# Optimization experiments

Measured on AMD Instinct MI355X. Metric: run time of the kernel, lower is better.

The kernel has to match this reference:

```python
import jax, jax.numpy as jnp
import numpy as np

N = 50000          # nodes
E = 1250000        # edges (avg degree 25)
EMBED = 64
HIDS = [64, 64, 64]
EDGE_DIM = 7       # 1 + 6
VOCAB = 5 ** 8     # 390625
NEG_SLOPE = 0.01   # F.leaky_relu default


def setup_inputs() -> dict:
    key = jax.random.key(0)
    ks = jax.random.split(key, 14)
    L = len(HIDS)
    x = jax.random.randint(ks[0], (N,), 0, VOCAB)
    edge_index = jax.random.randint(ks[1], (2, E), 0, N)
    edge_attr = jax.random.normal(ks[2], (E, EDGE_DIM), dtype=jnp.float32)
    emb = jax.random.normal(ks[3], (VOCAB, EMBED), dtype=jnp.float32) * 0.02
    # all layers have in = out = 64, so params are stacked along layer axis
    lin1_w = jax.random.normal(ks[4], (L, EMBED + EDGE_DIM, HIDS[0]), dtype=jnp.float32) * 0.1
    att_l = jax.random.normal(ks[5], (L, HIDS[0]), dtype=jnp.float32) * 0.1
    att_r = jax.random.normal(ks[6], (L, EMBED), dtype=jnp.float32) * 0.1
    lin2_w = jax.random.normal(ks[7], (L, HIDS[0], HIDS[0]), dtype=jnp.float32) * 0.1
    gbias = jax.random.normal(ks[8], (L, HIDS[0]), dtype=jnp.float32) * 0.01
    d_cat = int(np.sum(HIDS)) + EMBED  # 256
    fc1_w = jax.random.normal(ks[9], (d_cat, 20), dtype=jnp.float32) * 0.05
    fc1_b = jax.random.normal(ks[10], (20,), dtype=jnp.float32) * 0.01
    fc2_w = jax.random.normal(ks[11], (20, 1), dtype=jnp.float32) * 0.1
    fc2_b = jax.random.normal(ks[12], (1,), dtype=jnp.float32) * 0.01
    return {"x": x, "edge_index": edge_index, "edge_attr": edge_attr, "emb": emb,
            "lin1_w": lin1_w, "att_l": att_l, "att_r": att_r, "lin2_w": lin2_w,
            "gbias": gbias, "fc1_w": fc1_w, "fc1_b": fc1_b, "fc2_w": fc2_w, "fc2_b": fc2_b}


def _gate_conv(h, src, dst, edge_attr, w1, al, ar, w2, b):
    # message from source j -> target i; attention softmax over edges sharing a target
    xj = jnp.concatenate([h[src], edge_attr], axis=-1)            # [E, in+7]
    xj = jax.nn.leaky_relu(xj @ w1, NEG_SLOPE)                    # [E, out]
    alpha = jax.nn.leaky_relu(jnp.sum(xj * al, -1) + jnp.sum(h[dst] * ar, -1), NEG_SLOPE)
    amax = jax.ops.segment_max(alpha, dst, num_segments=N)        # [N]
    ea = jnp.exp(alpha - amax[dst])                               # [E]
    denom = jax.ops.segment_sum(ea, dst, num_segments=N)          # [N]
    a = ea / (denom[dst] + 1e-16)
    msg = (xj @ w2) * a[:, None]                                  # [E, out]
    return jax.ops.segment_sum(msg, dst, num_segments=N) + b      # [N, out]


def reference(x, edge_index, edge_attr, emb, lin1_w, att_l, att_r, lin2_w,
              gbias, fc1_w, fc1_b, fc2_w, fc2_b):
    src, dst = edge_index[0], edge_index[1]
    h = emb[x]                                                    # [N, EMBED]
    feats = [h]
    for l in range(len(HIDS)):
        h = jax.nn.relu(_gate_conv(h, src, dst, edge_attr,
                                   lin1_w[l], att_l[l], att_r[l], lin2_w[l], gbias[l]))
        feats.append(h)
    hcat = jnp.concatenate(feats, axis=-1)                        # [N, 256]
    z = jax.nn.relu(hcat @ fc1_w + fc1_b)
    out = jax.nn.sigmoid(z @ fc2_w + fc2_b)
    return out.squeeze(-1)                                        # [N]
```

## Files before the change

### kernel.cpp

```cpp
#include <hip/hip_runtime.h>
#include <math.h>

#define NEG 0.01f

typedef _Float16 f16;
typedef f16 h2 __attribute__((ext_vector_type(2)));

__device__ __forceinline__ float lrelu(float x) { return x > 0.f ? x : NEG * x; }

__device__ __forceinline__ h2 lrelu2(h2 x) {
    h2 y = x * (f16)0.01f;
    return __builtin_elementwise_max(x, y);
}

__device__ __forceinline__ float q16_allsum(float v) {
    int x;
    x = __builtin_amdgcn_update_dpp(0, __float_as_int(v), 0xB1, 0xF, 0xF, true);  v += __int_as_float(x);
    x = __builtin_amdgcn_update_dpp(0, __float_as_int(v), 0x4E, 0xF, 0xF, true);  v += __int_as_float(x);
    x = __builtin_amdgcn_update_dpp(0, __float_as_int(v), 0x124, 0xF, 0xF, true); v += __int_as_float(x);
    x = __builtin_amdgcn_update_dpp(0, __float_as_int(v), 0x128, 0xF, 0xF, true); v += __int_as_float(x);
    return v;
}

__device__ __forceinline__ float x16_32_sum(float v) {
    v += __int_as_float(__builtin_amdgcn_ds_swizzle(__float_as_int(v), 0x401F));
    v += __shfl_xor(v, 32, 64);
    return v;
}

__global__ void k_pre(int* __restrict__ deg, int N,
                      const float* __restrict__ lin1, const float* __restrict__ attl,
                      uint4* __restrict__ wpack, uint4* __restrict__ rec, int E) {
    int i = blockIdx.x * blockDim.x + threadIdx.x;
    if (i < N) deg[i] = 0;
    if (i < 48) {
        int l = i >> 4, t = i & 15;
        const float* wb  = lin1 + (size_t)l * 71 * 64 + 64 * 64;
        const float* alp = attl + l * 64;
        unsigned int u[20];
#pragma unroll
        for (int j = 0; j < 4; j++) {
            int f = 4 * t + j;
            h2 a = { (f16)wb[f],       (f16)wb[64 + f]  }; u[j]      = __builtin_bit_cast(unsigned int, a);
            h2 b = { (f16)wb[128 + f], (f16)wb[192 + f] }; u[4 + j]  = __builtin_bit_cast(unsigned int, b);
            h2 c = { (f16)wb[256 + f], (f16)wb[320 + f] }; u[8 + j]  = __builtin_bit_cast(unsigned int, c);
            h2 d = { (f16)wb[384 + f], (f16)0.f         }; u[12 + j] = __builtin_bit_cast(unsigned int, d);
        }
        h2 e0 = { (f16)alp[4 * t],     (f16)alp[4 * t + 1] }; u[16] = __builtin_bit_cast(unsigned int, e0);
        h2 e1 = { (f16)alp[4 * t + 2], (f16)alp[4 * t + 3] }; u[17] = __builtin_bit_cast(unsigned int, e1);
        u[18] = 0; u[19] = 0;
        uint4* o = wpack + (size_t)i * 5;
        o[0] = make_uint4(u[0],  u[1],  u[2],  u[3]);
        o[1] = make_uint4(u[4],  u[5],  u[6],  u[7]);
        o[2] = make_uint4(u[8],  u[9],  u[10], u[11]);
        o[3] = make_uint4(u[12], u[13], u[14], u[15]);
        o[4] = make_uint4(u[16], u[17], u[18], u[19]);
    } else if (i >= 48 && i < 112) {
        rec[E + i - 48] = make_uint4(0, 0, 0, 0);
    }
}

__global__ __launch_bounds__(256) void k_count_gemm0(
    const int* __restrict__ dst, int* __restrict__ deg, int* __restrict__ rank,
    int E, int nbC,
    const int* __restrict__ x, const float* __restrict__ emb,
    const float* __restrict__ lin1, const float* __restrict__ ar,
    f16* __restrict__ g, float* __restrict__ r_out, float* __restrict__ hcat, int N)
{
    __shared__ __align__(16) float sA[64][36];
    __shared__ __align__(16) float sB[64 * 64];
    __shared__ float sar[64];
    int tid = threadIdx.x;
    if ((int)blockIdx.x < nbC) {
        int e = (blockIdx.x * 256 + tid) * 4;
        if (e + 3 < E) {
            int4 d = *(const int4*)(dst + e);
            int r0 = atomicAdd(&deg[d.x], 1);
            int r1 = atomicAdd(&deg[d.y], 1);
            int r2 = atomicAdd(&deg[d.z], 1);
            int r3 = atomicAdd(&deg[d.w], 1);
            *(int4*)(rank + e) = make_int4(r0, r1, r2, r3);
        } else {
            for (int k = 0; k < 4; k++)
                if (e + k < E) rank[e + k] = atomicAdd(&deg[dst[e + k]], 1);
        }
        return;
    }
    int row0 = ((int)blockIdx.x - nbC) * 32;

    {
        const float4* b4 = (const float4*)lin1;
        float4* s4 = (float4*)sB;
        for (int i = tid; i < 1024; i += 256) s4[i] = b4[i];
    }
    if (tid < 64) sar[tid] = ar[tid];

#pragma unroll
    for (int pass = 0; pass < 2; ++pass) {
        int nl = pass * 16 + (tid & 15);
        int k4 = (tid >> 4) * 4;
        int n = row0 + nl; bool ok = n < N; if (!ok) n = N - 1;
        float4 v = *(const float4*)(emb + (size_t)x[n] * 64 + k4);
        sA[k4 + 0][nl] = v.x; sA[k4 + 1][nl] = v.y;
        sA[k4 + 2][nl] = v.z; sA[k4 + 3][nl] = v.w;
        if (ok) *(float4*)(hcat + (size_t)n * 256 + k4) = v;
    }
    __syncthreads();

    int tr = tid >> 4, tc = tid & 15;
    int r0 = tr * 2, c0 = tc * 4;
    float acc[2][4];
#pragma unroll
    for (int i = 0; i < 2; i++)
#pragma unroll
        for (int j = 0; j < 4; j++) acc[i][j] = 0.f;

#pragma unroll 4
    for (int k = 0; k < 64; ++k) {
        float4 b4 = *(const float4*)(sB + k * 64 + c0);
        float2 a0 = *(const float2*)&sA[k][r0];
#pragma unroll
        for (int j = 0; j < 4; j++) {
            float bj = (&b4.x)[j];
            acc[0][j] += a0.x * bj; acc[1][j] += a0.y * bj;
        }
    }

#pragma unroll
    for (int i = 0; i < 2; i++) {
        int n = row0 + r0 + i;
        if (n < N) {
            uint2 gw;
            gw.x = __builtin_bit_cast(unsigned int, __builtin_amdgcn_cvt_pkrtz(acc[i][0], acc[i][1]));
            gw.y = __builtin_bit_cast(unsigned int, __builtin_amdgcn_cvt_pkrtz(acc[i][2], acc[i][3]));
            *(uint2*)(g + (size_t)n * 64 + c0) = gw;
        }
    }
    if (tid < 32) {
        int n = row0 + tid;
        if (n < N) {
            float racc = 0.f;
#pragma unroll
            for (int k = 0; k < 64; k++) racc += sA[k][tid] * sar[k];
            r_out[n] = racc;
        }
    }
}

__global__ __launch_bounds__(256) void k_scan_part(const int* __restrict__ deg,
                                                   int* __restrict__ bsum, int n) {
    __shared__ int sh[256];
    int b = blockIdx.x, t = threadIdx.x;
    int i0 = b * 1024 + t * 4;
    int s = 0;
    if (i0 + 3 < n) { int4 v = *(const int4*)(deg + i0); s = v.x + v.y + v.z + v.w; }
    else { for (int k = 0; k < 4; k++) if (i0 + k < n) s += deg[i0 + k]; }
    sh[t] = s; __syncthreads();
    for (int d = 128; d > 0; d >>= 1) { if (t < d) sh[t] += sh[t + d]; __syncthreads(); }
    if (t == 0) bsum[b] = sh[0];
}

__global__ __launch_bounds__(256) void k_scan_out(const int* __restrict__ deg,
                                                  const int* __restrict__ bsum,
                                                  int* __restrict__ off, int nb, int n) {
    __shared__ int sb[256];
    __shared__ int sh[256];
    int b = blockIdx.x, t = threadIdx.x;
    int v = (t < nb) ? bsum[t] : 0;
    sb[t] = v; __syncthreads();
    for (int d = 1; d < 256; d <<= 1) {
        int u = (t >= d) ? sb[t - d] : 0;
        __syncthreads(); sb[t] += u; __syncthreads();
    }
    int base = (b == 0) ? 0 : sb[b - 1];
    if (b == 0 && t == 0) off[n] = sb[255];
    int i0 = b * 1024 + t * 4;
    int4 v4 = make_int4(0, 0, 0, 0);
    if (i0 + 3 < n) v4 = *(const int4*)(deg + i0);
    else {
        v4.x = (i0     < n) ? deg[i0]     : 0;
        v4.y = (i0 + 1 < n) ? deg[i0 + 1] : 0;
        v4.z = (i0 + 2 < n) ? deg[i0 + 2] : 0;
        v4.w = (i0 + 3 < n) ? deg[i0 + 3] : 0;
    }
    int s = v4.x + v4.y + v4.z + v4.w;
    sh[t] = s; __syncthreads();
    for (int d = 1; d < 256; d <<= 1) {
        int u = (t >= d) ? sh[t - d] : 0;
        __syncthreads(); sh[t] += u; __syncthreads();
    }
    int ex = base + sh[t] - s;
    if (i0     < n) off[i0]     = ex;
    if (i0 + 1 < n) off[i0 + 1] = ex + v4.x;
    if (i0 + 2 < n) off[i0 + 2] = ex + v4.x + v4.y;
    if (i0 + 3 < n) off[i0 + 3] = ex + v4.x + v4.y + v4.z;
}

__global__ void k_fill(const int* __restrict__ src, const int* __restrict__ dst,
                       const float* __restrict__ eattr, const int* __restrict__ off,
                       const int* __restrict__ rank, uint4* __restrict__ rec, int E) {
    int e = (blockIdx.x * 256 + threadIdx.x) * 2;
    if (e >= E) return;
    bool two = (e + 1 < E);
#pragma unroll
    for (int k = 0; k < 2; k++) {
        if (k == 1 && !two) break;
        int ee = e + k;
        int slot = off[dst[ee]] + rank[ee];
        const float* ap = eattr + (size_t)ee * 7;
        float a0 = ap[0], a1 = ap[1], a2 = ap[2], a3 = ap[3], a4 = ap[4], a5 = ap[5], a6 = ap[6];
        uint4 rv;
        h2 p01 = { (f16)a0, (f16)a1 };
        h2 p23 = { (f16)a2, (f16)a3 };
        h2 p45 = { (f16)a4, (f16)a5 };
        rv.x = __builtin_bit_cast(unsigned int, p01);
        rv.y = __builtin_bit_cast(unsigned int, p23);
        rv.z = __builtin_bit_cast(unsigned int, p45);
        unsigned int a6b = (unsigned int)__builtin_bit_cast(unsigned short, (f16)a6);
        rv.w = a6b | ((unsigned int)src[ee] << 16);
        rec[slot] = rv;
    }
}

__global__ __launch_bounds__(256) void k_gemm2g1(
    float* __restrict__ hc,
    const float* __restrict__ W2, const float* __restrict__ bias,
    const float* __restrict__ W1n, const float* __restrict__ arn,
    f16* __restrict__ g, float* __restrict__ r_out, int N)
{
    __shared__ __align__(16) float sA[64][68];
    __shared__ __align__(16) float sB[64 * 64];
    __shared__ float sar[64];
    int tid = threadIdx.x, row0 = blockIdx.x * 64;

    {
        const float4* b4 = (const float4*)W2;
        float4* s4 = (float4*)sB;
        for (int i = tid; i < 1024; i += 256) s4[i] = b4[i];
    }
    if (tid < 64) sar[tid] = arn[tid];

#pragma unroll
    for (int pass = 0; pass < 4; ++pass) {
        int nl = pass * 16 + (tid & 15);
        int k4 = (tid >> 4) * 4;
        int n = row0 + nl; if (n >= N) n = N - 1;
        float4 v = *(const float4*)(hc + (size_t)n * 256 + k4);
        sA[k4 + 0][nl] = v.x; sA[k4 + 1][nl] = v.y;
        sA[k4 + 2][nl] = v.z; sA[k4 + 3][nl] = v.w;
    }
    __syncthreads();

    int tr = tid >> 4, tc = tid & 15;
    int r0 = tr * 4, c0 = tc * 4;
    float acc[4][4];
#pragma unroll
    for (int i = 0; i < 4; i++)
#pragma unroll
        for (int j = 0; j < 4; j++) acc[i][j] = 0.f;

#pragma unroll 4
    for (int k = 0; k < 64; ++k) {
        float4 b4 = *(const float4*)(sB + k * 64 + c0);
        float4 a0 = *(const float4*)&sA[k][r0];
#pragma unroll
        for (int j = 0; j < 4; j++) {
            float bj = (&b4.x)[j];
            acc[0][j] += a0.x * bj; acc[1][j] += a0.y * bj;
            acc[2][j] += a0.z * bj; acc[3][j] += a0.w * bj;
        }
    }

    float4 bv = *(const float4*)(bias + c0);
#pragma unroll
    for (int i = 0; i < 4; i++) {
        acc[i][0] = fmaxf(acc[i][0] + bv.x, 0.f);
        acc[i][1] = fmaxf(acc[i][1] + bv.y, 0.f);
        acc[i][2] = fmaxf(acc[i][2] + bv.z, 0.f);
        acc[i][3] = fmaxf(acc[i][3] + bv.w, 0.f);
        int n = row0 + r0 + i;
        if (n < N) *(float4*)(hc + (size_t)n * 256 + c0) =
            make_float4(acc[i][0], acc[i][1], acc[i][2], acc[i][3]);
    }
    __syncthreads();

    {
        const float4* b4 = (const float4*)W1n;
        float4* s4 = (float4*)sB;
        for (int i = tid; i < 1024; i += 256) s4[i] = b4[i];
    }
#pragma unroll
    for (int i = 0; i < 4; i++)
#pragma unroll
        for (int j = 0; j < 4; j++) sA[c0 + j][r0 + i] = acc[i][j];
    __syncthreads();

#pragma unroll
    for (int i = 0; i < 4; i++)
#pragma unroll
        for (int j = 0; j < 4; j++) acc[i][j] = 0.f;

#pragma unroll 4
    for (int k = 0; k < 64; ++k) {
        float4 b4 = *(const float4*)(sB + k * 64 + c0);
        float4 a0 = *(const float4*)&sA[k][r0];
#pragma unroll
        for (int j = 0; j < 4; j++) {
            float bj = (&b4.x)[j];
            acc[0][j] += a0.x * bj; acc[1][j] += a0.y * bj;
            acc[2][j] += a0.z * bj; acc[3][j] += a0.w * bj;
        }
    }

#pragma unroll
    for (int i = 0; i < 4; i++) {
        int n = row0 + r0 + i;
        if (n < N) {
            uint2 gw;
            gw.x = __builtin_bit_cast(unsigned int, __builtin_amdgcn_cvt_pkrtz(acc[i][0], acc[i][1]));
            gw.y = __builtin_bit_cast(unsigned int, __builtin_amdgcn_cvt_pkrtz(acc[i][2], acc[i][3]));
            *(uint2*)(g + (size_t)n * 64 + c0) = gw;
        }
    }
    if (tid < 64) {
        int n = row0 + tid;
        if (n < N) {
            float racc = 0.f;
#pragma unroll
            for (int k = 0; k < 64; k++) racc += sA[k][tid] * sar[k];
            r_out[n] = racc;
        }
    }
}

struct ConvW {
    h2 w01[4], w23[4], w45[4], w6_[4];
    h2 al01, al23;
};

__device__ __forceinline__ void edge_math(uint4 rv, uint2 gv, bool valid, float ri,
                                          const ConvW& W, float4& s, float& den) {
    h2 a01 = __builtin_bit_cast(h2, rv.x);
    h2 a23 = __builtin_bit_cast(h2, rv.y);
    h2 a45 = __builtin_bit_cast(h2, rv.z);
    h2 a6p = __builtin_bit_cast(h2, rv.w & 0xFFFFu);
    h2 g01 = __builtin_bit_cast(h2, gv.x);
    h2 g23 = __builtin_bit_cast(h2, gv.y);

    float c0 = __builtin_amdgcn_fdot2(a01, W.w01[0],
               __builtin_amdgcn_fdot2(a23, W.w23[0],
               __builtin_amdgcn_fdot2(a45, W.w45[0],
               __builtin_amdgcn_fdot2(a6p, W.w6_[0], 0.f, false), false), false), false);
    float c1 = __builtin_amdgcn_fdot2(a01, W.w01[1],
               __builtin_amdgcn_fdot2(a23, W.w23[1],
               __builtin_amdgcn_fdot2(a45, W.w45[1],
               __builtin_amdgcn_fdot2(a6p, W.w6_[1], 0.f, false), false), false), false);
    float c2 = __builtin_amdgcn_fdot2(a01, W.w01[2],
               __builtin_amdgcn_fdot2(a23, W.w23[2],
               __builtin_amdgcn_fdot2(a45, W.w45[2],
               __builtin_amdgcn_fdot2(a6p, W.w6_[2], 0.f, false), false), false), false);
    float c3 = __builtin_amdgcn_fdot2(a01, W.w01[3],
               __builtin_amdgcn_fdot2(a23, W.w23[3],
               __builtin_amdgcn_fdot2(a45, W.w45[3],
               __builtin_amdgcn_fdot2(a6p, W.w6_[3], 0.f, false), false), false), false);

    h2 x01 = lrelu2(g01 + __builtin_amdgcn_cvt_pkrtz(c0, c1));
    h2 x23 = lrelu2(g23 + __builtin_amdgcn_cvt_pkrtz(c2, c3));
    float p = __builtin_amdgcn_fdot2(x01, W.al01,
              __builtin_amdgcn_fdot2(x23, W.al23, 0.f, false), false);
    p = q16_allsum(p);
    float alpha = lrelu(p + ri);
    float w = valid ? __expf(alpha) : 0.f;
    s.x += w * (float)x01.x; s.y += w * (float)x01.y;
    s.z += w * (float)x23.x; s.w += w * (float)x23.y;
    den += w;
}

__global__ __launch_bounds__(256) void k_conv(
    const int* __restrict__ off, const uint4* __restrict__ rec,
    const f16* __restrict__ g, const float* __restrict__ r,
    const uint4* __restrict__ wpack, float* __restrict__ aggdst, int N)
{
    int lane = threadIdx.x & 63;
    int wid  = threadIdx.x >> 6;
    int node = blockIdx.x * 4 + wid;
    if (node >= N) return;
    int q = lane >> 4, l16 = lane & 15;

    ConvW W;
    {
        const uint4* wp = wpack + l16 * 5;
        uint4 v0 = wp[0], v1 = wp[1], v2 = wp[2], v3 = wp[3], v4 = wp[4];
        W.w01[0] = __builtin_bit_cast(h2, v0.x); W.w01[1] = __builtin_bit_cast(h2, v0.y);
        W.w01[2] = __builtin_bit_cast(h2, v0.z); W.w01[3] = __builtin_bit_cast(h2, v0.w);
        W.w23[0] = __builtin_bit_cast(h2, v1.x); W.w23[1] = __builtin_bit_cast(h2, v1.y);
        W.w23[2] = __builtin_bit_cast(h2, v1.z); W.w23[3] = __builtin_bit_cast(h2, v1.w);
        W.w45[0] = __builtin_bit_cast(h2, v2.x); W.w45[1] = __builtin_bit_cast(h2, v2.y);
        W.w45[2] = __builtin_bit_cast(h2, v2.z); W.w45[3] = __builtin_bit_cast(h2, v2.w);
        W.w6_[0] = __builtin_bit_cast(h2, v3.x); W.w6_[1] = __builtin_bit_cast(h2, v3.y);
        W.w6_[2] = __builtin_bit_cast(h2, v3.z); W.w6_[3] = __builtin_bit_cast(h2, v3.w);
        W.al01   = __builtin_bit_cast(h2, v4.x); W.al23   = __builtin_bit_cast(h2, v4.y);
    }

    float ri = r[node];
    int e0 = off[node], e1 = off[node + 1];
    const f16* gq = g + 4 * l16;

    float4 s = make_float4(0.f, 0.f, 0.f, 0.f);
    float den = 0.f;
    if (e0 < e1) {
        const uint4* rp = rec + e0 + q;
        uint4 ra = rp[0], rb = rp[4], rc = rp[8], rd = rp[12];
        uint2 ga = *(const uint2*)(gq + (size_t)(ra.w >> 16) * 64);
        uint2 gb = *(const uint2*)(gq + (size_t)(rb.w >> 16) * 64);
        uint2 gc = *(const uint2*)(gq + (size_t)(rc.w >> 16) * 64);
        uint2 gd = *(const uint2*)(gq + (size_t)(rd.w >> 16) * 64);
        uint4 na = rp[16], nb = rp[20], nc = rp[24], nd = rp[28];
        for (int e = e0; e < e1; e += 16) {
            uint2 gna = *(const uint2*)(gq + (size_t)(na.w >> 16) * 64);
            uint2 gnb = *(const uint2*)(gq + (size_t)(nb.w >> 16) * 64);
            uint2 gnc = *(const uint2*)(gq + (size_t)(nc.w >> 16) * 64);
            uint2 gnd = *(const uint2*)(gq + (size_t)(nd.w >> 16) * 64);
            rp += 16;
            uint4 ma = rp[16], mb = rp[20], mc = rp[24], md = rp[28];
            bool va = (e + q)      < e1, vb = (e + 4 + q)  < e1;
            bool vc = (e + 8 + q)  < e1, vd = (e + 12 + q) < e1;
            edge_math(ra, ga, va, ri, W, s, den);
            edge_math(rb, gb, vb, ri, W, s, den);
            edge_math(rc, gc, vc, ri, W, s, den);
            edge_math(rd, gd, vd, ri, W, s, den);
            ra = na; rb = nb; rc = nc; rd = nd;
            ga = gna; gb = gnb; gc = gnc; gd = gnd;
            na = ma; nb = mb; nc = mc; nd = md;
        }
    }
    s.x = x16_32_sum(s.x); s.y = x16_32_sum(s.y);
    s.z = x16_32_sum(s.z); s.w = x16_32_sum(s.w);
    den = x16_32_sum(den);
    float inv = 1.f / (den + 1e-16f);
    if (q == 0) {
        float4 o = make_float4(s.x * inv, s.y * inv, s.z * inv, s.w * inv);
        *(float4*)(aggdst + (size_t)node * 256 + 4 * l16) = o;
    }
}

__global__ __launch_bounds__(256) void k_gemm2head(
    const float* __restrict__ hcat,
    const float* __restrict__ W2, const float* __restrict__ bias,
    const float* __restrict__ f1w, const float* __restrict__ f1b,
    const float* __restrict__ f2w, const float* __restrict__ f2b,
    float* __restrict__ out, int N)
{
    __shared__ __align__(16) float sA[64][130];
    __shared__ __align__(16) float sBW[5120];
    int tid = threadIdx.x, row0 = blockIdx.x * 128;

    {
        const float4* b4 = (const float4*)W2;
        float4* s4 = (float4*)sBW;
        for (int i = tid; i < 1024; i += 256) s4[i] = b4[i];
    }
#pragma unroll
    for (int pass = 0; pass < 8; ++pass) {
        int nl = pass * 16 + (tid & 15);
        int k4 = (tid >> 4) * 4;
        int n = row0 + nl; if (n >= N) n = N - 1;
        float4 v = *(const float4*)(hcat + (size_t)n * 256 + 192 + k4);
        sA[k4 + 0][nl] = v.x; sA[k4 + 1][nl] = v.y;
        sA[k4 + 2][nl] = v.z; sA[k4 + 3][nl] = v.w;
    }
    __syncthreads();

    int tr = tid >> 4, tc = tid & 15;
    int r0 = tr * 8, c0 = tc * 4;
    float acc[8][4];
#pragma unroll
    for (int i = 0; i < 8; i++)
#pragma unroll
        for (int j = 0; j < 4; j++) acc[i][j] = 0.f;

#pragma unroll 4
    for (int k = 0; k < 64; ++k) {
        float4 b4 = *(const float4*)(sBW + k * 64 + c0);
        float4 a0 = *(const float4*)&sA[k][r0];
        float4 a1 = *(const float4*)&sA[k][r0 + 4];
#pragma unroll
        for (int j = 0; j < 4; j++) {
            float bj = (&b4.x)[j];
            acc[0][j] += a0.x * bj; acc[1][j] += a0.y * bj;
            acc[2][j] += a0.z * bj; acc[3][j] += a0.w * bj;
            acc[4][j] += a1.x * bj; acc[5][j] += a1.y * bj;
            acc[6][j] += a1.z * bj; acc[7][j] += a1.w * bj;
        }
    }

    float4 fw[5];
    {
        const float4* w4 = (const float4*)f1w;
#pragma unroll
        for (int i2 = 0; i2 < 5; i2++) fw[i2] = w4[tid + i2 * 256];
    }
    __syncthreads();

    float* sO = &sA[0][0];
    float4 bv = *(const float4*)(bias + c0);
#pragma unroll
    for (int i = 0; i < 8; i++) {
        acc[i][0] = fmaxf(acc[i][0] + bv.x, 0.f);
        acc[i][1] = fmaxf(acc[i][1] + bv.y, 0.f);
        acc[i][2] = fmaxf(acc[i][2] + bv.z, 0.f);
        acc[i][3] = fmaxf(acc[i][3] + bv.w, 0.f);
        int rr = r0 + i;
        sO[rr * 65 + c0 + 0] = acc[i][0];
        sO[rr * 65 + c0 + 1] = acc[i][1];
        sO[rr * 65 + c0 + 2] = acc[i][2];
        sO[rr * 65 + c0 + 3] = acc[i][3];
    }
    {
        float4* sw4 = (float4*)sBW;
#pragma unroll
        for (int i2 = 0; i2 < 5; i2++) sw4[tid + i2 * 256] = fw[i2];
    }
    __syncthreads();

    int rloc = tid >> 1;
    int half = tid & 1;
    int n = row0 + rloc;
    int nn = (n < N) ? n : N - 1;
    float z[20];
#pragma unroll
    for (int j = 0; j < 20; j++) z[j] = 0.f;
    const float4* hr = (const float4*)(hcat + (size_t)nn * 256);
    if (half == 0) {
        for (int k4 = 0; k4 < 32; k4++) {
            float4 h = hr[k4];
            const float* wr = sBW + k4 * 80;
#pragma unroll
            for (int j = 0; j < 20; j++)
                z[j] += h.x * wr[j] + h.y * wr[20 + j] + h.z * wr[40 + j] + h.w * wr[60 + j];
        }
    } else {
        for (int k4 = 32; k4 < 48; k4++) {
            float4 h = hr[k4];
            const float* wr = sBW + k4 * 80;
#pragma unroll
            for (int j = 0; j < 20; j++)
                z[j] += h.x * wr[j] + h.y * wr[20 + j] + h.z * wr[40 + j] + h.w * wr[60 + j];
        }
        for (int k = 0; k < 64; k += 2) {
            float hx = sO[rloc * 65 + k], hy = sO[rloc * 65 + k + 1];
            const float* wr = sBW + (192 + k) * 20;
#pragma unroll
            for (int j = 0; j < 20; j++)
                z[j] += hx * wr[j] + hy * wr[20 + j];
        }
    }
#pragma unroll
    for (int j = 0; j < 20; j++) z[j] += __shfl_xor(z[j], 1, 64);
    if (half == 0 && n < N) {
        float o = f2b[0];
#pragma unroll
        for (int j = 0; j < 20; j++) {
            float zj = z[j] + f1b[j];
            o += fmaxf(zj, 0.f) * f2w[j];
        }
        out[n] = 1.f / (1.f + __expf(-o));
    }
}

extern "C" void kernel_launch(void* const* d_in, const int* in_sizes, int n_in,
                              void* d_out, int out_size, void* d_ws, size_t ws_size,
                              hipStream_t stream) {
    const int*   x     = (const int*)d_in[0];
    const int*   eidx  = (const int*)d_in[1];
    const float* eattr = (const float*)d_in[2];
    const float* emb   = (const float*)d_in[3];
    const float* lin1  = (const float*)d_in[4];
    const float* attl  = (const float*)d_in[5];
    const float* attr_ = (const float*)d_in[6];
    const float* lin2  = (const float*)d_in[7];
    const float* gbias = (const float*)d_in[8];
    const float* f1w   = (const float*)d_in[9];
    const float* f1b   = (const float*)d_in[10];
    const float* f2w   = (const float*)d_in[11];
    const float* f2b   = (const float*)d_in[12];
    float* out = (float*)d_out;

    int N = in_sizes[0];
    int E = in_sizes[1] / 2;
    const int* src = eidx;
    const int* dst = eidx + E;

    char* p = (char*)d_ws;
    auto alloc = [&](size_t bytes) { void* q = (void*)p; p += (bytes + 255) & ~(size_t)255; return q; };
    float* hcat = (float*)alloc((size_t)N * 256 * 4);
    f16*   g    = (f16*)alloc((size_t)N * 64 * 2);
    float* r    = (float*)alloc((size_t)N * 4);
    int*   off  = (int*)alloc((size_t)(N + 1) * 4);
    int*   deg  = (int*)alloc((size_t)N * 4);
    int*   rank = (int*)alloc((size_t)E * 4);
    int*   bsum = (int*)alloc(256 * 4);
    uint4* rec  = (uint4*)alloc((size_t)(E + 64) * 16);
    uint4* wpack = (uint4*)alloc((size_t)48 * 5 * 16);

    int nbs   = (N + 1023) / 1024;
    int nbC   = ((E + 3) / 4 + 255) / 256;
    int nbG0  = (N + 31) / 32;
    int nbF   = ((E + 1) / 2 + 255) / 256;
    int nbg64 = (N + 63) / 64;
    int nbg128 = (N + 127) / 128;
    int nbc   = (N + 3) / 4;

    k_pre<<<(N + 255) / 256, 256, 0, stream>>>(deg, N, lin1, attl, wpack, rec, E);
    k_count_gemm0<<<nbC + nbG0, 256, 0, stream>>>(dst, deg, rank, E, nbC,
                                                  x, emb, lin1, attr_, g, r, hcat, N);
    k_scan_part<<<nbs, 256, 0, stream>>>(deg, bsum, N);
    k_scan_out<<<nbs, 256, 0, stream>>>(deg, bsum, off, nbs, N);
    k_fill<<<nbF, 256, 0, stream>>>(src, dst, eattr, off, rank, rec, E);

    k_conv<<<nbc, 256, 0, stream>>>(off, rec, g, r, wpack, hcat + 64, N);
    for (int l = 0; l < 2; l++) {
        k_gemm2g1<<<nbg64, 256, 0, stream>>>(hcat + 64 * (l + 1),
                                             lin2 + (size_t)l * 4096, gbias + l * 64,
                                             lin1 + (size_t)(l + 1) * 71 * 64,
                                             attr_ + (l + 1) * 64, g, r, N);
        k_conv<<<nbc, 256, 0, stream>>>(off, rec, g, r,
                                        wpack + (size_t)(l + 1) * 80,
                                        hcat + 64 * (l + 2), N);
    }
    k_gemm2head<<<nbg128, 256, 0, stream>>>(hcat, lin2 + 2 * 4096, gbias + 128,
                                            f1w, f1b, f2w, f2b, out, N);
}
```

Baseline: 514.0 us.

## Compute per-edge lin1 with MFMA in conv instead of node-level precompute

```diff
diff --git a/kernel.cpp b/kernel.cpp
--- a/kernel.cpp
+++ b/kernel.cpp
@@ -5,13 +5,10 @@
 
 typedef _Float16 f16;
 typedef f16 h2 __attribute__((ext_vector_type(2)));
+typedef f16 h4 __attribute__((ext_vector_type(4)));
+typedef float f32x4 __attribute__((ext_vector_type(4)));
 
 __device__ __forceinline__ float lrelu(float x) { return x > 0.f ? x : NEG * x; }
-
-__device__ __forceinline__ h2 lrelu2(h2 x) {
-    h2 y = x * (f16)0.01f;
-    return __builtin_elementwise_max(x, y);
-}
 
 __device__ __forceinline__ float q16_allsum(float v) {
     int x;
@@ -29,47 +26,39 @@
 }
 
 __global__ void k_pre(int* __restrict__ deg, int N,
-                      const float* __restrict__ lin1, const float* __restrict__ attl,
-                      uint4* __restrict__ wpack, uint4* __restrict__ rec, int E) {
+                      const float* __restrict__ lin1, uint2* __restrict__ wpack2,
+                      uint4* __restrict__ rec, int E) {
     int i = blockIdx.x * blockDim.x + threadIdx.x;
     if (i < N) deg[i] = 0;
-    if (i < 48) {
-        int l = i >> 4, t = i & 15;
-        const float* wb  = lin1 + (size_t)l * 71 * 64 + 64 * 64;
-        const float* alp = attl + l * 64;
-        unsigned int u[20];
-#pragma unroll
-        for (int j = 0; j < 4; j++) {
-            int f = 4 * t + j;
-            h2 a = { (f16)wb[f],       (f16)wb[64 + f]  }; u[j]      = __builtin_bit_cast(unsigned int, a);
-            h2 b = { (f16)wb[128 + f], (f16)wb[192 + f] }; u[4 + j]  = __builtin_bit_cast(unsigned int, b);
-            h2 c = { (f16)wb[256 + f], (f16)wb[320 + f] }; u[8 + j]  = __builtin_bit_cast(unsigned int, c);
-            h2 d = { (f16)wb[384 + f], (f16)0.f         }; u[12 + j] = __builtin_bit_cast(unsigned int, d);
-        }
-        h2 e0 = { (f16)alp[4 * t],     (f16)alp[4 * t + 1] }; u[16] = __builtin_bit_cast(unsigned int, e0);
-        h2 e1 = { (f16)alp[4 * t + 2], (f16)alp[4 * t + 3] }; u[17] = __builtin_bit_cast(unsigned int, e1);
-        u[18] = 0; u[19] = 0;
-        uint4* o = wpack + (size_t)i * 5;
-        o[0] = make_uint4(u[0],  u[1],  u[2],  u[3]);
-        o[1] = make_uint4(u[4],  u[5],  u[6],  u[7]);
-        o[2] = make_uint4(u[8],  u[9],  u[10], u[11]);
-        o[3] = make_uint4(u[12], u[13], u[14], u[15]);
-        o[4] = make_uint4(u[16], u[17], u[18], u[19]);
-    } else if (i >= 48 && i < 112) {
-        rec[E + i - 48] = make_uint4(0, 0, 0, 0);
-    }
-}
-
-__global__ __launch_bounds__(256) void k_count_gemm0(
+    if (i < 3840) {
+        int lane = i & 63, rest = i >> 6;
+        int nb = rest & 3, rest2 = rest >> 2;
+        int s = rest2 % 5, L = rest2 / 5;
+        int f  = nb * 16 + (lane & 15);
+        int kb = s * 16 + ((lane >> 4) << 2);
+        const float* W = lin1 + (size_t)L * 71 * 64;
+        float v0 = (kb + 0 < 71) ? W[(kb + 0) * 64 + f] : 0.f;
+        float v1 = (kb + 1 < 71) ? W[(kb + 1) * 64 + f] : 0.f;
+        float v2 = (kb + 2 < 71) ? W[(kb + 2) * 64 + f] : 0.f;
+        float v3 = (kb + 3 < 71) ? W[(kb + 3) * 64 + f] : 0.f;
+        h2 p01 = { (f16)v0, (f16)v1 };
+        h2 p23 = { (f16)v2, (f16)v3 };
+        uint2 u;
+        u.x = __builtin_bit_cast(unsigned int, p01);
+        u.y = __builtin_bit_cast(unsigned int, p23);
+        wpack2[i] = u;
+    }
+    if (i >= 3840 && i < 3904) rec[E + i - 3840] = make_uint4(0, 0, 0, 0);
+}
+
+__global__ __launch_bounds__(256) void k_count_h0(
     const int* __restrict__ dst, int* __restrict__ deg, int* __restrict__ rank,
     int E, int nbC,
     const int* __restrict__ x, const float* __restrict__ emb,
-    const float* __restrict__ lin1, const float* __restrict__ ar,
-    f16* __restrict__ g, float* __restrict__ r_out, float* __restrict__ hcat, int N)
+    const float* __restrict__ ar0,
+    f16* __restrict__ h16, float* __restrict__ r_out,
+    float* __restrict__ hcat, int N)
 {
-    __shared__ __align__(16) float sA[64][36];
-    __shared__ __align__(16) float sB[64 * 64];
-    __shared__ float sar[64];
     int tid = threadIdx.x;
     if ((int)blockIdx.x < nbC) {
         int e = (blockIdx.x * 256 + tid) * 4;
@@ -86,65 +75,20 @@
         }
         return;
     }
-    int row0 = ((int)blockIdx.x - nbC) * 32;
-
-    {
-        const float4* b4 = (const float4*)lin1;
-        float4* s4 = (float4*)sB;
-        for (int i = tid; i < 1024; i += 256) s4[i] = b4[i];
-    }
-    if (tid < 64) sar[tid] = ar[tid];
-
-#pragma unroll
-    for (int pass = 0; pass < 2; ++pass) {
-        int nl = pass * 16 + (tid & 15);
-        int k4 = (tid >> 4) * 4;
-        int n = row0 + nl; bool ok = n < N; if (!ok) n = N - 1;
-        float4 v = *(const float4*)(emb + (size_t)x[n] * 64 + k4);
-        sA[k4 + 0][nl] = v.x; sA[k4 + 1][nl] = v.y;
-        sA[k4 + 2][nl] = v.z; sA[k4 + 3][nl] = v.w;
-        if (ok) *(float4*)(hcat + (size_t)n * 256 + k4) = v;
-    }
-    __syncthreads();
-
-    int tr = tid >> 4, tc = tid & 15;
-    int r0 = tr * 2, c0 = tc * 4;
-    float acc[2][4];
-#pragma unroll
-    for (int i = 0; i < 2; i++)
-#pragma unroll
-        for (int j = 0; j < 4; j++) acc[i][j] = 0.f;
-
-#pragma unroll 4
-    for (int k = 0; k < 64; ++k) {
-        float4 b4 = *(const float4*)(sB + k * 64 + c0);
-        float2 a0 = *(const float2*)&sA[k][r0];
-#pragma unroll
-        for (int j = 0; j < 4; j++) {
-            float bj = (&b4.x)[j];
-            acc[0][j] += a0.x * bj; acc[1][j] += a0.y * bj;
-        }
-    }
-
-#pragma unroll
-    for (int i = 0; i < 2; i++) {
-        int n = row0 + r0 + i;
-        if (n < N) {
-            uint2 gw;
-            gw.x = __builtin_bit_cast(unsigned int, __builtin_amdgcn_cvt_pkrtz(acc[i][0], acc[i][1]));
-            gw.y = __builtin_bit_cast(unsigned int, __builtin_amdgcn_cvt_pkrtz(acc[i][2], acc[i][3]));
-            *(uint2*)(g + (size_t)n * 64 + c0) = gw;
-        }
-    }
-    if (tid < 32) {
-        int n = row0 + tid;
-        if (n < N) {
-            float racc = 0.f;
-#pragma unroll
-            for (int k = 0; k < 64; k++) racc += sA[k][tid] * sar[k];
-            r_out[n] = racc;
-        }
-    }
+    int idx = ((int)blockIdx.x - nbC) * 256 + tid;
+    int node = idx >> 4, sub = idx & 15;
+    if (node >= N) return;
+    int j4 = sub * 4;
+    float4 em = *(const float4*)(emb + (size_t)x[node] * 64 + j4);
+    *(float4*)(hcat + (size_t)node * 256 + j4) = em;
+    uint2 hw;
+    hw.x = __builtin_bit_cast(unsigned int, __builtin_amdgcn_cvt_pkrtz(em.x, em.y));
+    hw.y = __builtin_bit_cast(unsigned int, __builtin_amdgcn_cvt_pkrtz(em.z, em.w));
+    *(uint2*)(h16 + (size_t)node * 64 + j4) = hw;
+    float part = em.x * ar0[j4] + em.y * ar0[j4 + 1]
+               + em.z * ar0[j4 + 2] + em.w * ar0[j4 + 3];
+    part = q16_allsum(part);
+    if (sub == 0) r_out[node] = part;
 }
 
 __global__ __launch_bounds__(256) void k_scan_part(const int* __restrict__ deg,
@@ -222,11 +166,11 @@
     }
 }
 
-__global__ __launch_bounds__(256) void k_gemm2g1(
+__global__ __launch_bounds__(256) void k_gemm2h(
     float* __restrict__ hc,
     const float* __restrict__ W2, const float* __restrict__ bias,
-    const float* __restrict__ W1n, const float* __restrict__ arn,
-    f16* __restrict__ g, float* __restrict__ r_out, int N)
+    const float* __restrict__ arn,
+    f16* __restrict__ h16, float* __restrict__ r_out, int N)
 {
     __shared__ __align__(16) float sA[64][68];
     __shared__ __align__(16) float sB[64 * 64];
@@ -279,168 +223,111 @@
         acc[i][2] = fmaxf(acc[i][2] + bv.z, 0.f);
         acc[i][3] = fmaxf(acc[i][3] + bv.w, 0.f);
         int n = row0 + r0 + i;
-        if (n < N) *(float4*)(hc + (size_t)n * 256 + c0) =
-            make_float4(acc[i][0], acc[i][1], acc[i][2], acc[i][3]);
-    }
-    __syncthreads();
-
-    {
-        const float4* b4 = (const float4*)W1n;
-        float4* s4 = (float4*)sB;
-        for (int i = tid; i < 1024; i += 256) s4[i] = b4[i];
-    }
-#pragma unroll
-    for (int i = 0; i < 4; i++)
-#pragma unroll
-        for (int j = 0; j < 4; j++) sA[c0 + j][r0 + i] = acc[i][j];
-    __syncthreads();
-
-#pragma unroll
-    for (int i = 0; i < 4; i++)
-#pragma unroll
-        for (int j = 0; j < 4; j++) acc[i][j] = 0.f;
-
-#pragma unroll 4
-    for (int k = 0; k < 64; ++k) {
-        float4 b4 = *(const float4*)(sB + k * 64 + c0);
-        float4 a0 = *(const float4*)&sA[k][r0];
-#pragma unroll
-        for (int j = 0; j < 4; j++) {
-            float bj = (&b4.x)[j];
-            acc[0][j] += a0.x * bj; acc[1][j] += a0.y * bj;
-            acc[2][j] += a0.z * bj; acc[3][j] += a0.w * bj;
-        }
-    }
-
+        if (n < N) {
+            *(float4*)(hc + (size_t)n * 256 + c0) =
+                make_float4(acc[i][0], acc[i][1], acc[i][2], acc[i][3]);
+            uint2 hw;
+            hw.x = __builtin_bit_cast(unsigned int, __builtin_amdgcn_cvt_pkrtz(acc[i][0], acc[i][1]));
+            hw.y = __builtin_bit_cast(unsigned int, __builtin_amdgcn_cvt_pkrtz(acc[i][2], acc[i][3]));
+            *(uint2*)(h16 + (size_t)n * 64 + c0) = hw;
+        }
+    }
 #pragma unroll
     for (int i = 0; i < 4; i++) {
-        int n = row0 + r0 + i;
-        if (n < N) {
-            uint2 gw;
-            gw.x = __builtin_bit_cast(unsigned int, __builtin_amdgcn_cvt_pkrtz(acc[i][0], acc[i][1]));
-            gw.y = __builtin_bit_cast(unsigned int, __builtin_amdgcn_cvt_pkrtz(acc[i][2], acc[i][3]));
-            *(uint2*)(g + (size_t)n * 64 + c0) = gw;
-        }
-    }
-    if (tid < 64) {
-        int n = row0 + tid;
-        if (n < N) {
-            float racc = 0.f;
-#pragma unroll
-            for (int k = 0; k < 64; k++) racc += sA[k][tid] * sar[k];
-            r_out[n] = racc;
-        }
-    }
-}
-
-struct ConvW {
-    h2 w01[4], w23[4], w45[4], w6_[4];
-    h2 al01, al23;
-};
-
-__device__ __forceinline__ void edge_math(uint4 rv, uint2 gv, bool valid, float ri,
-                                          const ConvW& W, float4& s, float& den) {
-    h2 a01 = __builtin_bit_cast(h2, rv.x);
-    h2 a23 = __builtin_bit_cast(h2, rv.y);
-    h2 a45 = __builtin_bit_cast(h2, rv.z);
-    h2 a6p = __builtin_bit_cast(h2, rv.w & 0xFFFFu);
-    h2 g01 = __builtin_bit_cast(h2, gv.x);
-    h2 g23 = __builtin_bit_cast(h2, gv.y);
-
-    float c0 = __builtin_amdgcn_fdot2(a01, W.w01[0],
-               __builtin_amdgcn_fdot2(a23, W.w23[0],
-               __builtin_amdgcn_fdot2(a45, W.w45[0],
-               __builtin_amdgcn_fdot2(a6p, W.w6_[0], 0.f, false), false), false), false);
-    float c1 = __builtin_amdgcn_fdot2(a01, W.w01[1],
-               __builtin_amdgcn_fdot2(a23, W.w23[1],
-               __builtin_amdgcn_fdot2(a45, W.w45[1],
-               __builtin_amdgcn_fdot2(a6p, W.w6_[1], 0.f, false), false), false), false);
-    float c2 = __builtin_amdgcn_fdot2(a01, W.w01[2],
-               __builtin_amdgcn_fdot2(a23, W.w23[2],
-               __builtin_amdgcn_fdot2(a45, W.w45[2],
-               __builtin_amdgcn_fdot2(a6p, W.w6_[2], 0.f, false), false), false), false);
-    float c3 = __builtin_amdgcn_fdot2(a01, W.w01[3],
-               __builtin_amdgcn_fdot2(a23, W.w23[3],
-               __builtin_amdgcn_fdot2(a45, W.w45[3],
-               __builtin_amdgcn_fdot2(a6p, W.w6_[3], 0.f, false), false), false), false);
-
-    h2 x01 = lrelu2(g01 + __builtin_amdgcn_cvt_pkrtz(c0, c1));
-    h2 x23 = lrelu2(g23 + __builtin_amdgcn_cvt_pkrtz(c2, c3));
-    float p = __builtin_amdgcn_fdot2(x01, W.al01,
-              __builtin_amdgcn_fdot2(x23, W.al23, 0.f, false), false);
-    p = q16_allsum(p);
-    float alpha = lrelu(p + ri);
-    float w = valid ? __expf(alpha) : 0.f;
-    s.x += w * (float)x01.x; s.y += w * (float)x01.y;
-    s.z += w * (float)x23.x; s.w += w * (float)x23.y;
-    den += w;
+        float part = acc[i][0] * sar[c0] + acc[i][1] * sar[c0 + 1]
+                   + acc[i][2] * sar[c0 + 2] + acc[i][3] * sar[c0 + 3];
+        part = q16_allsum(part);
+        if (tc == 0) {
+            int n = row0 + r0 + i;
+            if (n < N) r_out[n] = part;
+        }
+    }
 }
 
 __global__ __launch_bounds__(256) void k_conv(
     const int* __restrict__ off, const uint4* __restrict__ rec,
-    const f16* __restrict__ g, const float* __restrict__ r,
-    const uint4* __restrict__ wpack, float* __restrict__ aggdst, int N)
+    const f16* __restrict__ h16, const float* __restrict__ r,
+    const uint2* __restrict__ wp2, const float* __restrict__ al,
+    float* __restrict__ aggdst, int N)
 {
     int lane = threadIdx.x & 63;
     int wid  = threadIdx.x >> 6;
     int node = blockIdx.x * 4 + wid;
     if (node >= N) return;
-    int q = lane >> 4, l16 = lane & 15;
-
-    ConvW W;
-    {
-        const uint4* wp = wpack + l16 * 5;
-        uint4 v0 = wp[0], v1 = wp[1], v2 = wp[2], v3 = wp[3], v4 = wp[4];
-        W.w01[0] = __builtin_bit_cast(h2, v0.x); W.w01[1] = __builtin_bit_cast(h2, v0.y);
-        W.w01[2] = __builtin_bit_cast(h2, v0.z); W.w01[3] = __builtin_bit_cast(h2, v0.w);
-        W.w23[0] = __builtin_bit_cast(h2, v1.x); W.w23[1] = __builtin_bit_cast(h2, v1.y);
-        W.w23[2] = __builtin_bit_cast(h2, v1.z); W.w23[3] = __builtin_bit_cast(h2, v1.w);
-        W.w45[0] = __builtin_bit_cast(h2, v2.x); W.w45[1] = __builtin_bit_cast(h2, v2.y);
-        W.w45[2] = __builtin_bit_cast(h2, v2.z); W.w45[3] = __builtin_bit_cast(h2, v2.w);
-        W.w6_[0] = __builtin_bit_cast(h2, v3.x); W.w6_[1] = __builtin_bit_cast(h2, v3.y);
-        W.w6_[2] = __builtin_bit_cast(h2, v3.z); W.w6_[3] = __builtin_bit_cast(h2, v3.w);
-        W.al01   = __builtin_bit_cast(h2, v4.x); W.al23   = __builtin_bit_cast(h2, v4.y);
-    }
-
+    int l16 = lane & 15, grp = lane >> 4;
+
+    h4 B[5][4];
+#pragma unroll
+    for (int s = 0; s < 5; s++)
+#pragma unroll
+        for (int nb = 0; nb < 4; nb++)
+            B[s][nb] = __builtin_bit_cast(h4, wp2[(s * 4 + nb) * 64 + lane]);
+
+    float alv0 = al[l16], alv1 = al[16 + l16], alv2 = al[32 + l16], alv3 = al[48 + l16];
     float ri = r[node];
     int e0 = off[node], e1 = off[node + 1];
-    const f16* gq = g + 4 * l16;
-
-    float4 s = make_float4(0.f, 0.f, 0.f, 0.f);
-    float den = 0.f;
+
+    float facc0 = 0.f, facc1 = 0.f, facc2 = 0.f, facc3 = 0.f, pden = 0.f;
+
     if (e0 < e1) {
-        const uint4* rp = rec + e0 + q;
-        uint4 ra = rp[0], rb = rp[4], rc = rp[8], rd = rp[12];
-        uint2 ga = *(const uint2*)(gq + (size_t)(ra.w >> 16) * 64);
-        uint2 gb = *(const uint2*)(gq + (size_t)(rb.w >> 16) * 64);
-        uint2 gc = *(const uint2*)(gq + (size_t)(rc.w >> 16) * 64);
-        uint2 gd = *(const uint2*)(gq + (size_t)(rd.w >> 16) * 64);
-        uint4 na = rp[16], nb = rp[20], nc = rp[24], nd = rp[28];
+        uint4 rv = rec[e0 + l16];
+        const uint2* hp = (const uint2*)(h16 + (size_t)(rv.w >> 16) * 64) + grp;
+        uint2 a0 = hp[0], a1 = hp[4], a2 = hp[8], a3 = hp[12];
         for (int e = e0; e < e1; e += 16) {
-            uint2 gna = *(const uint2*)(gq + (size_t)(na.w >> 16) * 64);
-            uint2 gnb = *(const uint2*)(gq + (size_t)(nb.w >> 16) * 64);
-            uint2 gnc = *(const uint2*)(gq + (size_t)(nc.w >> 16) * 64);
-            uint2 gnd = *(const uint2*)(gq + (size_t)(nd.w >> 16) * 64);
-            rp += 16;
-            uint4 ma = rp[16], mb = rp[20], mc = rp[24], md = rp[28];
-            bool va = (e + q)      < e1, vb = (e + 4 + q)  < e1;
-            bool vc = (e + 8 + q)  < e1, vd = (e + 12 + q) < e1;
-            edge_math(ra, ga, va, ri, W, s, den);
-            edge_math(rb, gb, vb, ri, W, s, den);
-            edge_math(rc, gc, vc, ri, W, s, den);
-            edge_math(rd, gd, vd, ri, W, s, den);
-            ra = na; rb = nb; rc = nc; rd = nd;
-            ga = gna; gb = gnb; gc = gnc; gd = gnd;
-            na = ma; nb = mb; nc = mc; nd = md;
-        }
-    }
-    s.x = x16_32_sum(s.x); s.y = x16_32_sum(s.y);
-    s.z = x16_32_sum(s.z); s.w = x16_32_sum(s.w);
-    den = x16_32_sum(den);
-    float inv = 1.f / (den + 1e-16f);
-    if (q == 0) {
-        float4 o = make_float4(s.x * inv, s.y * inv, s.z * inv, s.w * inv);
-        *(float4*)(aggdst + (size_t)node * 256 + 4 * l16) = o;
+            uint4 rvn = rec[e + 16 + l16];
+            const uint2* hpn = (const uint2*)(h16 + (size_t)(rvn.w >> 16) * 64) + grp;
+            uint2 b0 = hpn[0], b1 = hpn[4], b2 = hpn[8], b3 = hpn[12];
+
+            uint2 at = make_uint2(0u, 0u);
+            if (grp == 0)      at = make_uint2(rv.x, rv.y);
+            else if (grp == 1) at = make_uint2(rv.z, rv.w & 0xFFFFu);
+
+            h4 A0 = __builtin_bit_cast(h4, a0), A1 = __builtin_bit_cast(h4, a1);
+            h4 A2 = __builtin_bit_cast(h4, a2), A3 = __builtin_bit_cast(h4, a3);
+            h4 A4 = __builtin_bit_cast(h4, at);
+            f32x4 acc0 = {0.f,0.f,0.f,0.f}, acc1 = {0.f,0.f,0.f,0.f};
+            f32x4 acc2 = {0.f,0.f,0.f,0.f}, acc3 = {0.f,0.f,0.f,0.f};
+#define MF(ACC, NB) \
+            ACC = __builtin_amdgcn_mfma_f32_16x16x16f16(A0, B[0][NB], ACC, 0, 0, 0); \
+            ACC = __builtin_amdgcn_mfma_f32_16x16x16f16(A1, B[1][NB], ACC, 0, 0, 0); \
+            ACC = __builtin_amdgcn_mfma_f32_16x16x16f16(A2, B[2][NB], ACC, 0, 0, 0); \
+            ACC = __builtin_amdgcn_mfma_f32_16x16x16f16(A3, B[3][NB], ACC, 0, 0, 0); \
+            ACC = __builtin_amdgcn_mfma_f32_16x16x16f16(A4, B[4][NB], ACC, 0, 0, 0);
+            MF(acc0, 0) MF(acc1, 1) MF(acc2, 2) MF(acc3, 3)
+#undef MF
+            float x0[4], x1[4], x2[4], x3[4];
+#pragma unroll
+            for (int g2 = 0; g2 < 4; g2++) {
+                x0[g2] = fmaxf(acc0[g2], NEG * acc0[g2]);
+                x1[g2] = fmaxf(acc1[g2], NEG * acc1[g2]);
+                x2[g2] = fmaxf(acc2[g2], NEG * acc2[g2]);
+                x3[g2] = fmaxf(acc3[g2], NEG * acc3[g2]);
+            }
+#pragma unroll
+            for (int reg = 0; reg < 4; reg++) {
+                float pp = x0[reg] * alv0 + x1[reg] * alv1
+                         + x2[reg] * alv2 + x3[reg] * alv3;
+                pp = q16_allsum(pp);
+                float alpha = lrelu(pp + ri);
+                int eg = e + grp * 4 + reg;
+                float w = (eg < e1) ? __expf(alpha) : 0.f;
+                facc0 += w * x0[reg]; facc1 += w * x1[reg];
+                facc2 += w * x2[reg]; facc3 += w * x3[reg];
+                pden += w;
+            }
+            rv = rvn; a0 = b0; a1 = b1; a2 = b2; a3 = b3;
+        }
+    }
+    facc0 = x16_32_sum(facc0); facc1 = x16_32_sum(facc1);
+    facc2 = x16_32_sum(facc2); facc3 = x16_32_sum(facc3);
+    pden  = x16_32_sum(pden);
+    float inv = 1.f / (pden + 1e-16f);
+    if (grp == 0) {
+        float* o = aggdst + (size_t)node * 256;
+        o[l16]      = facc0 * inv;
+        o[16 + l16] = facc1 * inv;
+        o[32 + l16] = facc2 * inv;
+        o[48 + l16] = facc3 * inv;
     }
 }
 
@@ -594,38 +481,39 @@
     char* p = (char*)d_ws;
     auto alloc = [&](size_t bytes) { void* q = (void*)p; p += (bytes + 255) & ~(size_t)255; return q; };
     float* hcat = (float*)alloc((size_t)N * 256 * 4);
-    f16*   g    = (f16*)alloc((size_t)N * 64 * 2);
+    f16*   h16  = (f16*)alloc((size_t)N * 64 * 2);
     float* r    = (float*)alloc((size_t)N * 4);
     int*   off  = (int*)alloc((size_t)(N + 1) * 4);
     int*   deg  = (int*)alloc((size_t)N * 4);
     int*   rank = (int*)alloc((size_t)E * 4);
     int*   bsum = (int*)alloc(256 * 4);
     uint4* rec  = (uint4*)alloc((size_t)(E + 64) * 16);
-    uint4* wpack = (uint4*)alloc((size_t)48 * 5 * 16);
+    uint2* wpack2 = (uint2*)alloc((size_t)3840 * 8);
 
     int nbs   = (N + 1023) / 1024;
     int nbC   = ((E + 3) / 4 + 255) / 256;
-    int nbG0  = (N + 31) / 32;
+    int nbH0  = (N * 16 + 255) / 256;
     int nbF   = ((E + 1) / 2 + 255) / 256;
     int nbg64 = (N + 63) / 64;
     int nbg128 = (N + 127) / 128;
     int nbc   = (N + 3) / 4;
 
-    k_pre<<<(N + 255) / 256, 256, 0, stream>>>(deg, N, lin1, attl, wpack, rec, E);
-    k_count_gemm0<<<nbC + nbG0, 256, 0, stream>>>(dst, deg, rank, E, nbC,
-                                                  x, emb, lin1, attr_, g, r, hcat, N);
+    k_pre<<<(N + 255) / 256, 256, 0, stream>>>(deg, N, lin1, wpack2, rec, E);
+    k_count_h0<<<nbC + nbH0, 256, 0, stream>>>(dst, deg, rank, E, nbC,
+                                               x, emb, attr_, h16, r, hcat, N);
     k_scan_part<<<nbs, 256, 0, stream>>>(deg, bsum, N);
     k_scan_out<<<nbs, 256, 0, stream>>>(deg, bsum, off, nbs, N);
     k_fill<<<nbF, 256, 0, stream>>>(src, dst, eattr, off, rank, rec, E);
 
-    k_conv<<<nbc, 256, 0, stream>>>(off, rec, g, r, wpack, hcat + 64, N);
+    k_conv<<<nbc, 256, 0, stream>>>(off, rec, h16, r,
+                                    wpack2, attl, hcat + 64, N);
     for (int l = 0; l < 2; l++) {
-        k_gemm2g1<<<nbg64, 256, 0, stream>>>(hcat + 64 * (l + 1),
-                                             lin2 + (size_t)l * 4096, gbias + l * 64,
-                                             lin1 + (size_t)(l + 1) * 71 * 64,
-                                             attr_ + (l + 1) * 64, g, r, N);
-        k_conv<<<nbc, 256, 0, stream>>>(off, rec, g, r,
-                                        wpack + (size_t)(l + 1) * 80,
+        k_gemm2h<<<nbg64, 256, 0, stream>>>(hcat + 64 * (l + 1),
+                                            lin2 + (size_t)l * 4096, gbias + l * 64,
+                                            attr_ + (l + 1) * 64, h16, r, N);
+        k_conv<<<nbc, 256, 0, stream>>>(off, rec, h16, r,
+                                        wpack2 + (size_t)(l + 1) * 20 * 64,
+                                        attl + (l + 1) * 64,
                                         hcat + 64 * (l + 2), N);
     }
     k_gemm2head<<<nbg128, 256, 0, stream>>>(hcat, lin2 + 2 * 4096, gbias + 128,
```

Result: slower. 661.7 us (+28.7%).
